# Kernel optimization log

Measured on AMD Instinct MI355X. Metric: run time of the kernel, lower is better.

## Reference

```python
import jax, jax.numpy as jnp
import numpy as np

B, T, D = 8, 1024, 768
H, HD = 12, 64
DFF = 3072
EPS = 1e-5


def setup_inputs() -> dict:
    key = jax.random.key(0)
    ks = jax.random.split(key, 6)
    s = lambda fan_in: 1.0 / np.sqrt(fan_in)
    return {
        "x": jax.random.normal(ks[0], (B, T, D), jnp.float32),
        "ln1_g": jnp.ones((D,), jnp.float32),
        "ln1_b": jnp.zeros((D,), jnp.float32),
        "w_qkv": jax.random.normal(ks[1], (D, 3 * D), jnp.float32) * s(D),
        "b_qkv": jnp.zeros((3 * D,), jnp.float32),
        "w_out": jax.random.normal(ks[2], (D, D), jnp.float32) * s(D),
        "b_out": jnp.zeros((D,), jnp.float32),
        "ln2_g": jnp.ones((D,), jnp.float32),
        "ln2_b": jnp.zeros((D,), jnp.float32),
        "w_fc1": jax.random.normal(ks[3], (D, DFF), jnp.float32) * s(D),
        "b_fc1": jnp.zeros((DFF,), jnp.float32),
        "w_fc2": jax.random.normal(ks[4], (DFF, D), jnp.float32) * s(DFF),
        "b_fc2": jnp.zeros((D,), jnp.float32),
    }


def _layernorm(x, g, b):
    mu = jnp.mean(x, axis=-1, keepdims=True)
    var = jnp.var(x, axis=-1, keepdims=True)
    return (x - mu) * jax.lax.rsqrt(var + EPS) * g + b


def reference(x, ln1_g, ln1_b, w_qkv, b_qkv, w_out, b_out,
              ln2_g, ln2_b, w_fc1, b_fc1, w_fc2, b_fc2):
    # --- attention branch (pre-norm) ---
    h = _layernorm(x, ln1_g, ln1_b)
    qkv = h @ w_qkv + b_qkv                      # [B,T,3D]
    q, k, v = jnp.split(qkv, 3, axis=-1)
    # [B,T,D] -> [B,H,T,HD]
    re = lambda t: t.reshape(B, T, H, HD).transpose(0, 2, 1, 3)
    q, k, v = re(q), re(k), re(v)
    scores = jnp.einsum("bhqd,bhkd->bhqk", q, k) * (1.0 / np.sqrt(HD))
    causal = jnp.tril(jnp.ones((T, T), bool))    # [T,T]
    scores = jnp.where(causal, scores, -jnp.inf)
    attn_weights = jax.nn.softmax(scores, axis=-1)  # [B,H,T,T]
    out = jnp.einsum("bhqk,bhkd->bhqd", attn_weights, v)
    out = out.transpose(0, 2, 1, 3).reshape(B, T, D)
    attn_out = out @ w_out + b_out
    x = x + attn_out
    # --- MLP branch (pre-norm) ---
    h2 = _layernorm(x, ln2_g, ln2_b)
    ff = jax.nn.gelu(h2 @ w_fc1 + b_fc1, approximate=False) @ w_fc2 + b_fc2
    x = x + ff
    return x, attn_weights
```

## Files before the change

kernel.cpp:

```cpp
#include <hip/hip_runtime.h>
#include <cstdint>
#include <cstddef>

namespace {

constexpr int Bb  = 8;
constexpr int Tt  = 1024;
constexpr int Dd  = 768;
constexpr int Hh  = 12;
constexpr int DFF = 3072;
constexpr int BT  = Bb * Tt;

typedef __attribute__((ext_vector_type(8))) short bf16x8;
typedef __attribute__((ext_vector_type(4))) short bf16x4;
typedef __attribute__((ext_vector_type(4))) float f32x4;

__device__ __forceinline__ short f2bf(float f) {
  union { float f; unsigned u; } v; v.f = f;
  unsigned r = v.u + 0x7fffu + ((v.u >> 16) & 1u);
  return (short)(r >> 16);
}
__device__ __forceinline__ float gelu_exact(float v) {
  return 0.5f * v * (1.0f + erff(v * 0.70710678118654752f));
}

#define MFMA16(a, b, c) __builtin_amdgcn_mfma_f32_16x16x32_bf16(a, b, c, 0, 0, 0)

__device__ __forceinline__ void gl_lds16(const short* g, short* l) {
  __builtin_amdgcn_global_load_lds(
      (const __attribute__((address_space(1))) unsigned int*)(g),
      (__attribute__((address_space(3))) unsigned int*)(l), 16, 0, 0);
}

__global__ __launch_bounds__(256) void cvt_t(const float* __restrict__ in,
                                             short* __restrict__ out,
                                             int K, int N) {
  __shared__ float tile[32][33];
  int k0 = blockIdx.x * 32, n0 = blockIdx.y * 32;
  int tx = threadIdx.x & 31, ty = threadIdx.x >> 5;
  #pragma unroll
  for (int r = ty; r < 32; r += 8)
    tile[r][tx] = in[(size_t)(k0 + r) * N + n0 + tx];
  __syncthreads();
  #pragma unroll
  for (int r = ty; r < 32; r += 8)
    out[(size_t)(n0 + r) * K + k0 + tx] = f2bf(tile[tx][r]);
}

__global__ __launch_bounds__(256) void ln_rows(const float* __restrict__ x,
                                               const float* __restrict__ g,
                                               const float* __restrict__ b,
                                               short* __restrict__ out) {
  int lane = threadIdx.x & 63, wid = threadIdx.x >> 6;
  int row = blockIdx.x * 4 + wid;
  const float* xr = x + (size_t)row * Dd;
  float v[12];
  float s = 0.f, ss = 0.f;
  #pragma unroll
  for (int c = 0; c < 3; c++) {
    float4 t = *(const float4*)&xr[c * 256 + lane * 4];
    v[c * 4 + 0] = t.x; v[c * 4 + 1] = t.y; v[c * 4 + 2] = t.z; v[c * 4 + 3] = t.w;
    s  += t.x + t.y + t.z + t.w;
    ss += t.x * t.x + t.y * t.y + t.z * t.z + t.w * t.w;
  }
  #pragma unroll
  for (int off = 1; off < 64; off <<= 1) {
    s += __shfl_xor(s, off); ss += __shfl_xor(ss, off);
  }
  float mu   = s * (1.f / Dd);
  float var  = ss * (1.f / Dd) - mu * mu;
  float rstd = rsqrtf(var + 1e-5f);
  #pragma unroll
  for (int c = 0; c < 3; c++) {
    bf16x4 o;
    #pragma unroll
    for (int j = 0; j < 4; j++) {
      int d = c * 256 + lane * 4 + j;
      o[j] = f2bf((v[c * 4 + j] - mu) * rstd * g[d] + b[d]);
    }
    *(bf16x4*)&out[(size_t)row * Dd + c * 256 + lane * 4] = o;
  }
}

template <int EPI, int N>
__global__ __launch_bounds__(256) void gemm_bt(const short* __restrict__ A,
                                               const short* __restrict__ Bt,
                                               const float* __restrict__ bias,
                                               const float* __restrict__ add,
                                               void* __restrict__ outp,
                                               int K) {
  __shared__ short S[17408];
  short* As0 = S;
  short* As1 = S + 4096;
  short* Bs0 = S + 8192;
  short* Bs1 = S + 12288;

  int nbx = gridDim.x;
  int flat = blockIdx.y * nbx + blockIdx.x;
  int cpx = (nbx * gridDim.y) >> 3;
  int swz = (flat & 7) * cpx + (flat >> 3);
  int m0 = (swz % nbx) * 128, n0 = (swz / nbx) * 128;

  int tid = threadIdx.x;
  int lane = tid & 63, wid = tid >> 6;
  int wm = wid >> 1, wn = wid & 1;
  int l15 = lane & 15, lg = lane >> 4;

  int jr = tid >> 2, jc = (tid & 3) << 3;
  int ldsb = wid << 9;

  auto stage = [&](short* Ad, short* Bd, int k0) {
    gl_lds16(&A[(size_t)(m0 + jr) * K + k0 + jc],       Ad + ldsb);
    gl_lds16(&A[(size_t)(m0 + 64 + jr) * K + k0 + jc],  Ad + 2048 + ldsb);
    gl_lds16(&Bt[(size_t)(n0 + jr) * K + k0 + jc],      Bd + ldsb);
    gl_lds16(&Bt[(size_t)(n0 + 64 + jr) * K + k0 + jc], Bd + 2048 + ldsb);
  };

  f32x4 acc[4][4] = {};
  stage(As0, Bs0, 0);
  int nk = K >> 5;
  for (int t = 0; t < nk; ++t) {
    short* Ab = (t & 1) ? As1 : As0;
    short* Bb = (t & 1) ? Bs1 : Bs0;
    if (t + 1 < nk) {
      stage((t & 1) ? As0 : As1, (t & 1) ? Bs0 : Bs1, (t + 1) << 5);
      asm volatile("s_waitcnt vmcnt(4)" ::: "memory");
    } else {
      asm volatile("s_waitcnt vmcnt(0)" ::: "memory");
    }
    __syncthreads();
    bf16x8 af[4], bfr[4];
    #pragma unroll
    for (int i = 0; i < 4; i++) af[i]  = *(bf16x8*)&Ab[(wm * 64 + i * 16 + l15) * 32 + lg * 8];
    #pragma unroll
    for (int j = 0; j < 4; j++) bfr[j] = *(bf16x8*)&Bb[(wn * 64 + j * 16 + l15) * 32 + lg * 8];
    #pragma unroll
    for (int i = 0; i < 4; i++)
      #pragma unroll
      for (int j = 0; j < 4; j++)
        acc[i][j] = MFMA16(af[i], bfr[j], acc[i][j]);
    __syncthreads();
  }

  if (EPI == 0 || EPI == 2) {
    short (*Cl)[136] = (short (*)[136])S;
    #pragma unroll
    for (int i = 0; i < 4; i++)
      #pragma unroll
      for (int j = 0; j < 4; j++)
        #pragma unroll
        for (int r = 0; r < 4; r++) {
          int row = wm * 64 + i * 16 + lg * 4 + r;
          int col = wn * 64 + j * 16 + l15;
          float vv = acc[i][j][r] + bias[n0 + col];
          if (EPI == 2) vv = gelu_exact(vv);
          int ch = col >> 3, co = col & 7;
          Cl[row][((ch ^ (row & 7)) << 3) | co] = f2bf(vv);
        }
    __syncthreads();
    int row = tid >> 1;
    int cb = (tid & 1) * 8;
    #pragma unroll
    for (int c = 0; c < 8; c++) {
      int ch = cb + c;
      bf16x8 v8 = *(bf16x8*)&Cl[row][(ch ^ (row & 7)) << 3];
      *(bf16x8*)&((short*)outp)[(size_t)(m0 + row) * N + n0 + (ch << 3)] = v8;
    }
  } else {
    #pragma unroll
    for (int i = 0; i < 4; i++)
      #pragma unroll
      for (int j = 0; j < 4; j++)
        #pragma unroll
        for (int r = 0; r < 4; r++) {
          int m = m0 + wm * 64 + i * 16 + lg * 4 + r;
          int n = n0 + wn * 64 + j * 16 + l15;
          float vv = acc[i][j][r] + bias[n];
          size_t idx = (size_t)m * N + n;
          float ov = vv + add[idx];
          if (EPI == 3) __builtin_nontemporal_store(ov, &((float*)outp)[idx]);
          else          ((float*)outp)[idx] = ov;
        }
  }
}

__global__ __launch_bounds__(256) void attn_fused(const short* __restrict__ qkv,
                                                  float* __restrict__ attw,
                                                  short* __restrict__ ctx) {
  __shared__ short Vt[64][72];
  __shared__ float Pf[4][16][68];
  int flat = blockIdx.y * 16 + blockIdx.x;
  int xcd = flat & 7, rr0 = flat >> 3;
  int bh   = xcd * 12 + (rr0 >> 4);
  int tile = 15 - (rr0 & 15);
  int q0 = tile * 64;
  int b = bh / Hh, h = bh % Hh;
  int tid = threadIdx.x, lane = tid & 63, wid = tid >> 6;
  int l15 = lane & 15, lg = lane >> 4;
  const short* base = qkv + (size_t)b * Tt * 2304;

  bf16x8 qa[2];
  {
    const short* qp = base + (size_t)(q0 + wid * 16 + l15) * 2304 + h * 64 + lg * 8;
    qa[0] = *(const bf16x8*)qp;
    qa[1] = *(const bf16x8*)(qp + 32);
  }

  float l[4] = {0.f, 0.f, 0.f, 0.f};
  for (int kt = 0; kt <= tile; ++kt) {
    f32x4 acc[4] = {};
    #pragma unroll
    for (int nf = 0; nf < 4; ++nf) {
      const short* kp = base + (size_t)(kt * 64 + nf * 16 + l15) * 2304 + 768 + h * 64 + lg * 8;
      bf16x8 k0 = *(const bf16x8*)kp;
      bf16x8 k1 = *(const bf16x8*)(kp + 32);
      acc[nf] = MFMA16(qa[0], k0, acc[nf]);
      acc[nf] = MFMA16(qa[1], k1, acc[nf]);
    }
    #pragma unroll
    for (int r = 0; r < 4; r++) {
      int qg = q0 + wid * 16 + lg * 4 + r;
      #pragma unroll
      for (int nf = 0; nf < 4; nf++) {
        int kg = kt * 64 + nf * 16 + l15;
        l[r] += (kg <= qg) ? __expf(acc[nf][r] * 0.125f) : 0.f;
      }
    }
  }
  float rl[4];
  #pragma unroll
  for (int r = 0; r < 4; r++) {
    float s = l[r];
    #pragma unroll
    for (int off = 1; off < 16; off <<= 1) s += __shfl_xor(s, off);
    rl[r] = 1.f / s;
  }

  f32x4 oacc[4] = {};
  for (int kt = 0; kt <= tile; ++kt) {
    __syncthreads();
    {
      int t = tid & 63, dv = (tid >> 6) * 16;
      const short* vp = base + (size_t)(kt * 64 + t) * 2304 + 1536 + h * 64 + dv;
      bf16x8 v0 = *(const bf16x8*)vp;
      bf16x8 v1 = *(const bf16x8*)(vp + 8);
      #pragma unroll
      for (int j = 0; j < 8; j++) Vt[dv + j][t] = v0[j];
      #pragma unroll
      for (int j = 0; j < 8; j++) Vt[dv + 8 + j][t] = v1[j];
    }
    __syncthreads();

    f32x4 acc[4] = {};
    #pragma unroll
    for (int nf = 0; nf < 4; nf++) {
      const short* kp = base + (size_t)(kt * 64 + nf * 16 + l15) * 2304 + 768 + h * 64 + lg * 8;
      bf16x8 k0 = *(const bf16x8*)kp;
      bf16x8 k1 = *(const bf16x8*)(kp + 32);
      acc[nf] = MFMA16(qa[0], k0, acc[nf]);
      acc[nf] = MFMA16(qa[1], k1, acc[nf]);
    }
    #pragma unroll
    for (int nf = 0; nf < 4; nf++) {
      #pragma unroll
      for (int r = 0; r < 4; r++) {
        int qg = q0 + wid * 16 + lg * 4 + r;
        int kg = kt * 64 + nf * 16 + l15;
        float p = (kg <= qg) ? __expf(acc[nf][r] * 0.125f) * rl[r] : 0.f;
        Pf[wid][lg * 4 + r][nf * 16 + l15] = p;
      }
    }
    asm volatile("s_waitcnt lgkmcnt(0)" ::: "memory");
    __builtin_amdgcn_sched_barrier(0);
    #pragma unroll
    for (int it = 0; it < 4; ++it) {
      int pr = it * 4 + lg;
      f32x4 pv = *(f32x4*)&Pf[wid][pr][l15 * 4];
      __builtin_nontemporal_store(
          pv, (f32x4*)&attw[((size_t)bh * Tt + q0 + wid * 16 + pr) * Tt + kt * 64 + l15 * 4]);
    }
    f32x4 pf0 = *(f32x4*)&Pf[wid][l15][lg * 8];
    f32x4 pf1 = *(f32x4*)&Pf[wid][l15][lg * 8 + 4];
    f32x4 pf2 = *(f32x4*)&Pf[wid][l15][lg * 8 + 32];
    f32x4 pf3 = *(f32x4*)&Pf[wid][l15][lg * 8 + 36];
    bf16x8 pa0, pa1;
    #pragma unroll
    for (int j = 0; j < 4; j++) {
      pa0[j] = f2bf(pf0[j]); pa0[4 + j] = f2bf(pf1[j]);
      pa1[j] = f2bf(pf2[j]); pa1[4 + j] = f2bf(pf3[j]);
    }
    #pragma unroll
    for (int nf = 0; nf < 4; nf++) {
      bf16x8 vb0 = *(bf16x8*)&Vt[nf * 16 + l15][lg * 8];
      bf16x8 vb1 = *(bf16x8*)&Vt[nf * 16 + l15][lg * 8 + 32];
      oacc[nf] = MFMA16(pa0, vb0, oacc[nf]);
      oacc[nf] = MFMA16(pa1, vb1, oacc[nf]);
    }
  }
  f32x4 z = {0.f, 0.f, 0.f, 0.f};
  for (int kt = tile + 1; kt < 16; ++kt) {
    #pragma unroll
    for (int it = 0; it < 4; ++it) {
      int pr = it * 4 + lg;
      __builtin_nontemporal_store(
          z, (f32x4*)&attw[((size_t)bh * Tt + q0 + wid * 16 + pr) * Tt + kt * 64 + l15 * 4]);
    }
  }
  #pragma unroll
  for (int nf = 0; nf < 4; nf++) {
    #pragma unroll
    for (int r = 0; r < 4; r++) {
      int t = q0 + wid * 16 + lg * 4 + r;
      ctx[((size_t)b * Tt + t) * Dd + h * 64 + nf * 16 + l15] = f2bf(oacc[nf][r]);
    }
  }
}

}

extern "C" void kernel_launch(void* const* d_in, const int* in_sizes, int n_in,
                              void* d_out, int out_size, void* d_ws, size_t ws_size,
                              hipStream_t stream) {
  const float* x     = (const float*)d_in[0];
  const float* ln1g  = (const float*)d_in[1];
  const float* ln1b  = (const float*)d_in[2];
  const float* w_qkv = (const float*)d_in[3];
  const float* b_qkv = (const float*)d_in[4];
  const float* w_out = (const float*)d_in[5];
  const float* b_out = (const float*)d_in[6];
  const float* ln2g  = (const float*)d_in[7];
  const float* ln2b  = (const float*)d_in[8];
  const float* w_fc1 = (const float*)d_in[9];
  const float* b_fc1 = (const float*)d_in[10];
  const float* w_fc2 = (const float*)d_in[11];
  const float* b_fc2 = (const float*)d_in[12];

  char* ws = (char*)d_ws;
  size_t o = 0;
  short* wqkvT = (short*)(ws + o); o += (size_t)2304 * 768 * 2;
  short* woutT = (short*)(ws + o); o += (size_t)768 * 768 * 2;
  short* wfc1T = (short*)(ws + o); o += (size_t)3072 * 768 * 2;
  short* wfc2T = (short*)(ws + o); o += (size_t)768 * 3072 * 2;
  short* h     = (short*)(ws + o); o += (size_t)BT * Dd * 2;
  short* qkv   = (short*)(ws + o); o += (size_t)BT * 2304 * 2;
  float* y1    = (float*)(ws + o); o += (size_t)BT * Dd * 4;
  short* h2    = (short*)(ws + o); o += (size_t)BT * Dd * 2;
  short* ctx  = h;
  short* gbuf = h;

  float* out_x = (float*)d_out;
  float* attw  = out_x + (size_t)BT * Dd;

  cvt_t<<<dim3(768 / 32, 2304 / 32), 256, 0, stream>>>(w_qkv, wqkvT, 768, 2304);
  cvt_t<<<dim3(768 / 32, 768 / 32),  256, 0, stream>>>(w_out, woutT, 768, 768);
  cvt_t<<<dim3(768 / 32, 3072 / 32), 256, 0, stream>>>(w_fc1, wfc1T, 768, 3072);
  cvt_t<<<dim3(3072 / 32, 768 / 32), 256, 0, stream>>>(w_fc2, wfc2T, 3072, 768);

  ln_rows<<<BT / 4, 256, 0, stream>>>(x, ln1g, ln1b, h);
  gemm_bt<0, 2304><<<dim3(BT / 128, 2304 / 128), 256, 0, stream>>>(h, wqkvT, b_qkv, nullptr, qkv, 768);
  attn_fused<<<dim3(16, 96), 256, 0, stream>>>(qkv, attw, ctx);
  gemm_bt<1, 768><<<dim3(BT / 128, 768 / 128), 256, 0, stream>>>(ctx, woutT, b_out, x, y1, 768);
  ln_rows<<<BT / 4, 256, 0, stream>>>(y1, ln2g, ln2b, h2);
  gemm_bt<2, 3072><<<dim3(BT / 128, 3072 / 128), 256, 0, stream>>>(h2, wfc1T, b_fc1, nullptr, gbuf, 768);
  gemm_bt<3, 768><<<dim3(BT / 128, 768 / 128), 256, 0, stream>>>(gbuf, wfc2T, b_fc2, y1, out_x, 3072);
}
```

Baseline: 441.7 us.

## Add 256x256-tile 512-thread GEMM for QKV and FC1 projections

Adds a new GEMM kernel with 256x256 output tiles, 8 waves, a K-step of 64, double-buffered direct global-to-LDS loads with XOR swizzle, and a two-pass epilogue staged through LDS. It replaces the 128x128 kernel for the QKV and FC1 projections. The aim is more data reuse per LDS load and fewer global loads per FLOP. The cost is 128 KB of LDS per block and a large accumulator register footprint, and the grids are smaller (288 and 384 blocks), which may hurt wave balance across the CUs. The old bf16-output epilogue path is removed from gemm_bt.

```diff
diff --git a/kernel.cpp b/kernel.cpp
--- a/kernel.cpp
+++ b/kernel.cpp
@@ -25,6 +25,8 @@
 }
 
 #define MFMA16(a, b, c) __builtin_amdgcn_mfma_f32_16x16x32_bf16(a, b, c, 0, 0, 0)
+#define WAITV(n) asm volatile("s_waitcnt vmcnt(" #n ")" ::: "memory")
+#define BARRIER() asm volatile("s_barrier" ::: "memory")
 
 __device__ __forceinline__ void gl_lds16(const short* g, short* l) {
   __builtin_amdgcn_global_load_lds(
@@ -79,6 +81,106 @@
       o[j] = f2bf((v[c * 4 + j] - mu) * rstd * g[d] + b[d]);
     }
     *(bf16x4*)&out[(size_t)row * Dd + c * 256 + lane * 4] = o;
+  }
+}
+
+template <int EPI>
+__global__ __launch_bounds__(512, 2) void gemm256(const short* __restrict__ A,
+                                                  const short* __restrict__ Bt,
+                                                  const float* __restrict__ bias,
+                                                  short* __restrict__ outp,
+                                                  int N, int K) {
+  __shared__ short S[65536];
+  int nbx = gridDim.x;
+  int flat = blockIdx.y * nbx + blockIdx.x;
+  int cpx = (nbx * gridDim.y) >> 3;
+  int swz = (flat & 7) * cpx + (flat >> 3);
+  int m0 = (swz % nbx) * 256, n0 = (swz / nbx) * 256;
+
+  int tid = threadIdx.x;
+  int lane = tid & 63, wid = tid >> 6;
+  int wm = wid >> 2, wn = wid & 3;
+  int l15 = lane & 15, lg = lane >> 4;
+
+  int srow = wid * 8 + (lane >> 3);
+  int gslot = (lane & 7) ^ (srow & 7);
+
+  auto stage = [&](int dbuf, int kt) {
+    int dst = dbuf * 32768 + (wid << 9);
+    #pragma unroll
+    for (int p = 0; p < 4; ++p) {
+      const short* g = (p < 2)
+        ? &A [(size_t)(m0 + (p & 1) * 128 + srow) * K + kt * 64 + gslot * 8]
+        : &Bt[(size_t)(n0 + (p & 1) * 128 + srow) * K + kt * 64 + gslot * 8];
+      gl_lds16(g, &S[dst + p * 8192]);
+      gl_lds16(g + (size_t)64 * K, &S[dst + p * 8192 + 4096]);
+    }
+  };
+
+  f32x4 acc[8][4] = {};
+  stage(0, 0);
+  int NT = K >> 6;
+  for (int kt = 0; kt < NT; ++kt) {
+    int d = kt & 1;
+    if (kt + 1 < NT) {
+      stage(d ^ 1, kt + 1);
+      WAITV(8);
+    } else {
+      WAITV(0);
+    }
+    BARRIER();
+
+    const int bB = d * 32768 + 16384 + (wn >> 1) * 8192;
+    bf16x8 rB[8];
+    #pragma unroll
+    for (int n = 0; n < 4; n++) {
+      int r = (wn & 1) * 64 + n * 16 + l15;
+      rB[n * 2 + 0] = *(const bf16x8*)&S[bB + r * 64 + (((lg    ) ^ (r & 7)) << 3)];
+      rB[n * 2 + 1] = *(const bf16x8*)&S[bB + r * 64 + (((4 + lg) ^ (r & 7)) << 3)];
+    }
+    const int bA = d * 32768 + wm * 8192;
+    #pragma unroll
+    for (int m = 0; m < 8; m++) {
+      int r = m * 16 + l15;
+      bf16x8 a0 = *(const bf16x8*)&S[bA + r * 64 + (((lg    ) ^ (r & 7)) << 3)];
+      bf16x8 a1 = *(const bf16x8*)&S[bA + r * 64 + (((4 + lg) ^ (r & 7)) << 3)];
+      #pragma unroll
+      for (int n = 0; n < 4; n++) {
+        acc[m][n] = MFMA16(a0, rB[n * 2 + 0], acc[m][n]);
+        acc[m][n] = MFMA16(a1, rB[n * 2 + 1], acc[m][n]);
+      }
+    }
+    BARRIER();
+  }
+
+  __syncthreads();
+  #pragma unroll
+  for (int ch = 0; ch < 2; ++ch) {
+    if (wm == ch) {
+      #pragma unroll
+      for (int m = 0; m < 8; m++)
+        #pragma unroll
+        for (int n = 0; n < 4; n++) {
+          int col = wn * 64 + n * 16 + l15;
+          float bs = bias[n0 + col];
+          #pragma unroll
+          for (int r = 0; r < 4; r++) {
+            int row = m * 16 + lg * 4 + r;
+            float vv = acc[m][n][r] + bs;
+            if (EPI == 2) vv = gelu_exact(vv);
+            S[row * 256 + ((((col >> 3) ^ (row & 7)) << 3) | (col & 7))] = f2bf(vv);
+          }
+        }
+    }
+    __syncthreads();
+    int row = tid >> 2;
+    #pragma unroll
+    for (int c = 0; c < 8; c++) {
+      int cc = (tid & 3) + c * 4;
+      bf16x8 v8 = *(bf16x8*)&S[row * 256 + ((cc ^ (row & 7)) << 3)];
+      *(bf16x8*)&outp[(size_t)(m0 + ch * 128 + row) * N + n0 + cc * 8] = v8;
+    }
+    __syncthreads();
   }
 }
 
@@ -142,46 +244,20 @@
     __syncthreads();
   }
 
-  if (EPI == 0 || EPI == 2) {
-    short (*Cl)[136] = (short (*)[136])S;
-    #pragma unroll
-    for (int i = 0; i < 4; i++)
-      #pragma unroll
-      for (int j = 0; j < 4; j++)
-        #pragma unroll
-        for (int r = 0; r < 4; r++) {
-          int row = wm * 64 + i * 16 + lg * 4 + r;
-          int col = wn * 64 + j * 16 + l15;
-          float vv = acc[i][j][r] + bias[n0 + col];
-          if (EPI == 2) vv = gelu_exact(vv);
-          int ch = col >> 3, co = col & 7;
-          Cl[row][((ch ^ (row & 7)) << 3) | co] = f2bf(vv);
-        }
-    __syncthreads();
-    int row = tid >> 1;
-    int cb = (tid & 1) * 8;
-    #pragma unroll
-    for (int c = 0; c < 8; c++) {
-      int ch = cb + c;
-      bf16x8 v8 = *(bf16x8*)&Cl[row][(ch ^ (row & 7)) << 3];
-      *(bf16x8*)&((short*)outp)[(size_t)(m0 + row) * N + n0 + (ch << 3)] = v8;
-    }
-  } else {
-    #pragma unroll
-    for (int i = 0; i < 4; i++)
-      #pragma unroll
-      for (int j = 0; j < 4; j++)
-        #pragma unroll
-        for (int r = 0; r < 4; r++) {
-          int m = m0 + wm * 64 + i * 16 + lg * 4 + r;
-          int n = n0 + wn * 64 + j * 16 + l15;
-          float vv = acc[i][j][r] + bias[n];
-          size_t idx = (size_t)m * N + n;
-          float ov = vv + add[idx];
-          if (EPI == 3) __builtin_nontemporal_store(ov, &((float*)outp)[idx]);
-          else          ((float*)outp)[idx] = ov;
-        }
-  }
+  #pragma unroll
+  for (int i = 0; i < 4; i++)
+    #pragma unroll
+    for (int j = 0; j < 4; j++)
+      #pragma unroll
+      for (int r = 0; r < 4; r++) {
+        int m = m0 + wm * 64 + i * 16 + lg * 4 + r;
+        int n = n0 + wn * 64 + j * 16 + l15;
+        float vv = acc[i][j][r] + bias[n];
+        size_t idx = (size_t)m * N + n;
+        float ov = vv + add[idx];
+        if (EPI == 3) __builtin_nontemporal_store(ov, &((float*)outp)[idx]);
+        else          ((float*)outp)[idx] = ov;
+      }
 }
 
 __global__ __launch_bounds__(256) void attn_fused(const short* __restrict__ qkv,
@@ -357,10 +433,10 @@
   cvt_t<<<dim3(3072 / 32, 768 / 32), 256, 0, stream>>>(w_fc2, wfc2T, 3072, 768);
 
   ln_rows<<<BT / 4, 256, 0, stream>>>(x, ln1g, ln1b, h);
-  gemm_bt<0, 2304><<<dim3(BT / 128, 2304 / 128), 256, 0, stream>>>(h, wqkvT, b_qkv, nullptr, qkv, 768);
+  gemm256<0><<<dim3(BT / 256, 2304 / 256), 512, 0, stream>>>(h, wqkvT, b_qkv, qkv, 2304, 768);
   attn_fused<<<dim3(16, 96), 256, 0, stream>>>(qkv, attw, ctx);
   gemm_bt<1, 768><<<dim3(BT / 128, 768 / 128), 256, 0, stream>>>(ctx, woutT, b_out, x, y1, 768);
   ln_rows<<<BT / 4, 256, 0, stream>>>(y1, ln2g, ln2b, h2);
-  gemm_bt<2, 3072><<<dim3(BT / 128, 3072 / 128), 256, 0, stream>>>(h2, wfc1T, b_fc1, nullptr, gbuf, 768);
+  gemm256<2><<<dim3(BT / 256, DFF / 256), 512, 0, stream>>>(h2, wfc1T, b_fc1, gbuf, DFF, 768);
   gemm_bt<3, 768><<<dim3(BT / 128, 768 / 128), 256, 0, stream>>>(gbuf, wfc2T, b_fc2, y1, out_x, 3072);
 }
```

New measurement: 490.5 us. 1.11x slower.

## Split fused attention into context kernel and attention-weights kernel

Applied to the files above, without the earlier changes.

The single attention kernel made two passes: one to compute softmax row sums and one to write the weights and accumulate P·V. It now becomes two kernels. attn_ctx makes one pass, accumulating unnormalized P·V together with the row sums, normalizing at the end and saving the sums to workspace. attn_w then recomputes QK^T and writes the normalized weights. Total QK^T work stays about the same, but the compute-heavy P·V path no longer shares a kernel with the bandwidth-heavy weight stores. The cost is an extra launch and a small sums buffer, and exp is applied without max subtraction (as before).

```diff
diff --git a/kernel.cpp b/kernel.cpp
--- a/kernel.cpp
+++ b/kernel.cpp
@@ -184,9 +184,9 @@
   }
 }
 
-__global__ __launch_bounds__(256) void attn_fused(const short* __restrict__ qkv,
-                                                  float* __restrict__ attw,
-                                                  short* __restrict__ ctx) {
+__global__ __launch_bounds__(256) void attn_ctx(const short* __restrict__ qkv,
+                                                float* __restrict__ sums,
+                                                short* __restrict__ ctx) {
   __shared__ short Vt[64][72];
   __shared__ float Pf[4][16][68];
   int flat = blockIdx.y * 16 + blockIdx.x;
@@ -207,35 +207,6 @@
   }
 
   float l[4] = {0.f, 0.f, 0.f, 0.f};
-  for (int kt = 0; kt <= tile; ++kt) {
-    f32x4 acc[4] = {};
-    #pragma unroll
-    for (int nf = 0; nf < 4; ++nf) {
-      const short* kp = base + (size_t)(kt * 64 + nf * 16 + l15) * 2304 + 768 + h * 64 + lg * 8;
-      bf16x8 k0 = *(const bf16x8*)kp;
-      bf16x8 k1 = *(const bf16x8*)(kp + 32);
-      acc[nf] = MFMA16(qa[0], k0, acc[nf]);
-      acc[nf] = MFMA16(qa[1], k1, acc[nf]);
-    }
-    #pragma unroll
-    for (int r = 0; r < 4; r++) {
-      int qg = q0 + wid * 16 + lg * 4 + r;
-      #pragma unroll
-      for (int nf = 0; nf < 4; nf++) {
-        int kg = kt * 64 + nf * 16 + l15;
-        l[r] += (kg <= qg) ? __expf(acc[nf][r] * 0.125f) : 0.f;
-      }
-    }
-  }
-  float rl[4];
-  #pragma unroll
-  for (int r = 0; r < 4; r++) {
-    float s = l[r];
-    #pragma unroll
-    for (int off = 1; off < 16; off <<= 1) s += __shfl_xor(s, off);
-    rl[r] = 1.f / s;
-  }
-
   f32x4 oacc[4] = {};
   for (int kt = 0; kt <= tile; ++kt) {
     __syncthreads();
@@ -266,8 +237,96 @@
       for (int r = 0; r < 4; r++) {
         int qg = q0 + wid * 16 + lg * 4 + r;
         int kg = kt * 64 + nf * 16 + l15;
-        float p = (kg <= qg) ? __expf(acc[nf][r] * 0.125f) * rl[r] : 0.f;
+        float p = (kg <= qg) ? __expf(acc[nf][r] * 0.125f) : 0.f;
         Pf[wid][lg * 4 + r][nf * 16 + l15] = p;
+        l[r] += p;
+      }
+    }
+    asm volatile("s_waitcnt lgkmcnt(0)" ::: "memory");
+    __builtin_amdgcn_sched_barrier(0);
+    f32x4 pf0 = *(f32x4*)&Pf[wid][l15][lg * 8];
+    f32x4 pf1 = *(f32x4*)&Pf[wid][l15][lg * 8 + 4];
+    f32x4 pf2 = *(f32x4*)&Pf[wid][l15][lg * 8 + 32];
+    f32x4 pf3 = *(f32x4*)&Pf[wid][l15][lg * 8 + 36];
+    bf16x8 pa0, pa1;
+    #pragma unroll
+    for (int j = 0; j < 4; j++) {
+      pa0[j] = f2bf(pf0[j]); pa0[4 + j] = f2bf(pf1[j]);
+      pa1[j] = f2bf(pf2[j]); pa1[4 + j] = f2bf(pf3[j]);
+    }
+    #pragma unroll
+    for (int nf = 0; nf < 4; nf++) {
+      bf16x8 vb0 = *(bf16x8*)&Vt[nf * 16 + l15][lg * 8];
+      bf16x8 vb1 = *(bf16x8*)&Vt[nf * 16 + l15][lg * 8 + 32];
+      oacc[nf] = MFMA16(pa0, vb0, oacc[nf]);
+      oacc[nf] = MFMA16(pa1, vb1, oacc[nf]);
+    }
+  }
+  float rl[4];
+  #pragma unroll
+  for (int r = 0; r < 4; r++) {
+    #pragma unroll
+    for (int off = 1; off < 16; off <<= 1) l[r] += __shfl_xor(l[r], off);
+    rl[r] = 1.f / l[r];
+  }
+  #pragma unroll
+  for (int nf = 0; nf < 4; nf++) {
+    #pragma unroll
+    for (int r = 0; r < 4; r++) {
+      int t = q0 + wid * 16 + lg * 4 + r;
+      ctx[((size_t)b * Tt + t) * Dd + h * 64 + nf * 16 + l15] = f2bf(oacc[nf][r] * rl[r]);
+    }
+  }
+  if (l15 == 0) {
+    #pragma unroll
+    for (int r = 0; r < 4; r++)
+      sums[(size_t)bh * Tt + q0 + wid * 16 + lg * 4 + r] = l[r];
+  }
+}
+
+__global__ __launch_bounds__(256) void attn_w(const short* __restrict__ qkv,
+                                              const float* __restrict__ sums,
+                                              float* __restrict__ attw) {
+  __shared__ float Pf[4][16][68];
+  int flat = blockIdx.y * 16 + blockIdx.x;
+  int xcd = flat & 7, rr0 = flat >> 3;
+  int bh   = xcd * 12 + (rr0 >> 4);
+  int tile = 15 - (rr0 & 15);
+  int q0 = tile * 64;
+  int b = bh / Hh, h = bh % Hh;
+  int tid = threadIdx.x, lane = tid & 63, wid = tid >> 6;
+  int l15 = lane & 15, lg = lane >> 4;
+  const short* base = qkv + (size_t)b * Tt * 2304;
+
+  bf16x8 qa[2];
+  {
+    const short* qp = base + (size_t)(q0 + wid * 16 + l15) * 2304 + h * 64 + lg * 8;
+    qa[0] = *(const bf16x8*)qp;
+    qa[1] = *(const bf16x8*)(qp + 32);
+  }
+  float rl[4];
+  #pragma unroll
+  for (int r = 0; r < 4; r++)
+    rl[r] = 1.f / sums[(size_t)bh * Tt + q0 + wid * 16 + lg * 4 + r];
+
+  for (int kt = 0; kt <= tile; ++kt) {
+    f32x4 acc[4] = {};
+    #pragma unroll
+    for (int nf = 0; nf < 4; nf++) {
+      const short* kp = base + (size_t)(kt * 64 + nf * 16 + l15) * 2304 + 768 + h * 64 + lg * 8;
+      bf16x8 k0 = *(const bf16x8*)kp;
+      bf16x8 k1 = *(const bf16x8*)(kp + 32);
+      acc[nf] = MFMA16(qa[0], k0, acc[nf]);
+      acc[nf] = MFMA16(qa[1], k1, acc[nf]);
+    }
+    #pragma unroll
+    for (int nf = 0; nf < 4; nf++) {
+      #pragma unroll
+      for (int r = 0; r < 4; r++) {
+        int qg = q0 + wid * 16 + lg * 4 + r;
+        int kg = kt * 64 + nf * 16 + l15;
+        Pf[wid][lg * 4 + r][nf * 16 + l15] =
+            (kg <= qg) ? __expf(acc[nf][r] * 0.125f) * rl[r] : 0.f;
       }
     }
     asm volatile("s_waitcnt lgkmcnt(0)" ::: "memory");
@@ -279,23 +338,6 @@
       __builtin_nontemporal_store(
           pv, (f32x4*)&attw[((size_t)bh * Tt + q0 + wid * 16 + pr) * Tt + kt * 64 + l15 * 4]);
     }
-    f32x4 pf0 = *(f32x4*)&Pf[wid][l15][lg * 8];
-    f32x4 pf1 = *(f32x4*)&Pf[wid][l15][lg * 8 + 4];
-    f32x4 pf2 = *(f32x4*)&Pf[wid][l15][lg * 8 + 32];
-    f32x4 pf3 = *(f32x4*)&Pf[wid][l15][lg * 8 + 36];
-    bf16x8 pa0, pa1;
-    #pragma unroll
-    for (int j = 0; j < 4; j++) {
-      pa0[j] = f2bf(pf0[j]); pa0[4 + j] = f2bf(pf1[j]);
-      pa1[j] = f2bf(pf2[j]); pa1[4 + j] = f2bf(pf3[j]);
-    }
-    #pragma unroll
-    for (int nf = 0; nf < 4; nf++) {
-      bf16x8 vb0 = *(bf16x8*)&Vt[nf * 16 + l15][lg * 8];
-      bf16x8 vb1 = *(bf16x8*)&Vt[nf * 16 + l15][lg * 8 + 32];
-      oacc[nf] = MFMA16(pa0, vb0, oacc[nf]);
-      oacc[nf] = MFMA16(pa1, vb1, oacc[nf]);
-    }
   }
   f32x4 z = {0.f, 0.f, 0.f, 0.f};
   for (int kt = tile + 1; kt < 16; ++kt) {
@@ -304,14 +346,6 @@
       int pr = it * 4 + lg;
       __builtin_nontemporal_store(
           z, (f32x4*)&attw[((size_t)bh * Tt + q0 + wid * 16 + pr) * Tt + kt * 64 + l15 * 4]);
-    }
-  }
-  #pragma unroll
-  for (int nf = 0; nf < 4; nf++) {
-    #pragma unroll
-    for (int r = 0; r < 4; r++) {
-      int t = q0 + wid * 16 + lg * 4 + r;
-      ctx[((size_t)b * Tt + t) * Dd + h * 64 + nf * 16 + l15] = f2bf(oacc[nf][r]);
     }
   }
 }
@@ -345,6 +379,7 @@
   short* qkv   = (short*)(ws + o); o += (size_t)BT * 2304 * 2;
   float* y1    = (float*)(ws + o); o += (size_t)BT * Dd * 4;
   short* h2    = (short*)(ws + o); o += (size_t)BT * Dd * 2;
+  float* sums  = (float*)(ws + o); o += (size_t)96 * Tt * 4;
   short* ctx  = h;
   short* gbuf = h;
 
@@ -358,7 +393,8 @@
 
   ln_rows<<<BT / 4, 256, 0, stream>>>(x, ln1g, ln1b, h);
   gemm_bt<0, 2304><<<dim3(BT / 128, 2304 / 128), 256, 0, stream>>>(h, wqkvT, b_qkv, nullptr, qkv, 768);
-  attn_fused<<<dim3(16, 96), 256, 0, stream>>>(qkv, attw, ctx);
+  attn_ctx<<<dim3(16, 96), 256, 0, stream>>>(qkv, sums, ctx);
+  attn_w<<<dim3(16, 96), 256, 0, stream>>>(qkv, sums, attw);
   gemm_bt<1, 768><<<dim3(BT / 128, 768 / 128), 256, 0, stream>>>(ctx, woutT, b_out, x, y1, 768);
   ln_rows<<<BT / 4, 256, 0, stream>>>(y1, ln2g, ln2b, h2);
   gemm_bt<2, 3072><<<dim3(BT / 128, 3072 / 128), 256, 0, stream>>>(h2, wfc1T, b_fc1, nullptr, gbuf, 768);
```

Result: slower. 480.4 us (+8.8%).

## Pre-transpose V and double-buffer it into LDS via async loads

Applied to the files above, without the earlier changes.

Adds a separate kernel that transposes V per head into a contiguous [bh][d][t] workspace buffer. The attention kernel then stages the next V tile into a swizzled double-buffered LDS array with direct global-to-LDS loads, overlapped with the current tile's QK/softmax work. This replaces per-iteration scalar transposing stores and two block barriers. It costs an extra kernel launch and an extra round trip of V through global memory, and it relies on the gl_lds16 helper and a hand-written vmcnt wait being correct.

```diff
diff --git a/kernel.cpp b/kernel.cpp
--- a/kernel.cpp
+++ b/kernel.cpp
@@ -80,6 +80,28 @@
     }
     *(bf16x4*)&out[(size_t)row * Dd + c * 256 + lane * 4] = o;
   }
+}
+
+__global__ __launch_bounds__(256) void vtr(const short* __restrict__ qkv,
+                                           short* __restrict__ vt) {
+  __shared__ short Ts[64][72];
+  int bh = blockIdx.x, t0 = blockIdx.y * 64;
+  int b = bh / Hh, h = bh % Hh;
+  int tid = threadIdx.x;
+  int r = tid >> 2, dc = (tid & 3) * 16;
+  const short* vp = qkv + (size_t)b * Tt * 2304 + (size_t)(t0 + r) * 2304 + 1536 + h * 64 + dc;
+  bf16x8 v0 = *(const bf16x8*)vp;
+  bf16x8 v1 = *(const bf16x8*)(vp + 8);
+  *(bf16x8*)&Ts[r][dc] = v0;
+  *(bf16x8*)&Ts[r][dc + 8] = v1;
+  __syncthreads();
+  int d = tid >> 2, tc = (tid & 3) * 16;
+  bf16x8 o0, o1;
+  #pragma unroll
+  for (int j = 0; j < 8; j++) { o0[j] = Ts[tc + j][d]; o1[j] = Ts[tc + 8 + j][d]; }
+  short* op = vt + ((size_t)bh * 64 + d) * Tt + t0 + tc;
+  *(bf16x8*)op = o0;
+  *(bf16x8*)(op + 8) = o1;
 }
 
 template <int EPI, int N>
@@ -185,9 +207,10 @@
 }
 
 __global__ __launch_bounds__(256) void attn_fused(const short* __restrict__ qkv,
+                                                  const short* __restrict__ vt,
                                                   float* __restrict__ attw,
                                                   short* __restrict__ ctx) {
-  __shared__ short Vt[64][72];
+  __shared__ short VtL[2][4096];
   __shared__ float Pf[4][16][68];
   int flat = blockIdx.y * 16 + blockIdx.x;
   int xcd = flat & 7, rr0 = flat >> 3;
@@ -236,21 +259,18 @@
     rl[r] = 1.f / s;
   }
 
+  const short* vtb = vt + (size_t)bh * 64 * Tt;
+  int dS = wid * 16 + (lane >> 3);
+  int cS = (lane & 7) ^ (lane >> 3);
+  auto stageV = [&](int bi, int kt) {
+    gl_lds16(&vtb[(size_t)dS * Tt + kt * 64 + cS * 8],       &VtL[bi][wid * 1024]);
+    gl_lds16(&vtb[(size_t)(dS + 8) * Tt + kt * 64 + cS * 8], &VtL[bi][wid * 1024 + 512]);
+  };
+
   f32x4 oacc[4] = {};
+  stageV(0, 0);
   for (int kt = 0; kt <= tile; ++kt) {
-    __syncthreads();
-    {
-      int t = tid & 63, dv = (tid >> 6) * 16;
-      const short* vp = base + (size_t)(kt * 64 + t) * 2304 + 1536 + h * 64 + dv;
-      bf16x8 v0 = *(const bf16x8*)vp;
-      bf16x8 v1 = *(const bf16x8*)(vp + 8);
-      #pragma unroll
-      for (int j = 0; j < 8; j++) Vt[dv + j][t] = v0[j];
-      #pragma unroll
-      for (int j = 0; j < 8; j++) Vt[dv + 8 + j][t] = v1[j];
-    }
-    __syncthreads();
-
+    int cur = kt & 1;
     f32x4 acc[4] = {};
     #pragma unroll
     for (int nf = 0; nf < 4; nf++) {
@@ -289,10 +309,16 @@
       pa0[j] = f2bf(pf0[j]); pa0[4 + j] = f2bf(pf1[j]);
       pa1[j] = f2bf(pf2[j]); pa1[4 + j] = f2bf(pf3[j]);
     }
+    asm volatile("s_waitcnt vmcnt(4)" ::: "memory");
+    __builtin_amdgcn_s_barrier();
+    __builtin_amdgcn_sched_barrier(0);
+    if (kt < tile) stageV(cur ^ 1, kt + 1);
     #pragma unroll
     for (int nf = 0; nf < 4; nf++) {
-      bf16x8 vb0 = *(bf16x8*)&Vt[nf * 16 + l15][lg * 8];
-      bf16x8 vb1 = *(bf16x8*)&Vt[nf * 16 + l15][lg * 8 + 32];
+      int dA = nf * 16 + l15;
+      int sw = dA & 7;
+      bf16x8 vb0 = *(bf16x8*)&VtL[cur][dA * 64 + ((lg ^ sw) << 3)];
+      bf16x8 vb1 = *(bf16x8*)&VtL[cur][dA * 64 + (((4 + lg) ^ sw) << 3)];
       oacc[nf] = MFMA16(pa0, vb0, oacc[nf]);
       oacc[nf] = MFMA16(pa1, vb1, oacc[nf]);
     }
@@ -345,6 +371,7 @@
   short* qkv   = (short*)(ws + o); o += (size_t)BT * 2304 * 2;
   float* y1    = (float*)(ws + o); o += (size_t)BT * Dd * 4;
   short* h2    = (short*)(ws + o); o += (size_t)BT * Dd * 2;
+  short* vt    = (short*)(ws + o); o += (size_t)96 * 64 * Tt * 2;
   short* ctx  = h;
   short* gbuf = h;
 
@@ -358,7 +385,8 @@
 
   ln_rows<<<BT / 4, 256, 0, stream>>>(x, ln1g, ln1b, h);
   gemm_bt<0, 2304><<<dim3(BT / 128, 2304 / 128), 256, 0, stream>>>(h, wqkvT, b_qkv, nullptr, qkv, 768);
-  attn_fused<<<dim3(16, 96), 256, 0, stream>>>(qkv, attw, ctx);
+  vtr<<<dim3(96, 16), 256, 0, stream>>>(qkv, vt);
+  attn_fused<<<dim3(16, 96), 256, 0, stream>>>(qkv, vt, attw, ctx);
   gemm_bt<1, 768><<<dim3(BT / 128, 768 / 128), 256, 0, stream>>>(ctx, woutT, b_out, x, y1, 768);
   ln_rows<<<BT / 4, 256, 0, stream>>>(y1, ln2g, ln2b, h2);
   gemm_bt<2, 3072><<<dim3(BT / 128, 3072 / 128), 256, 0, stream>>>(h2, wfc1T, b_fc1, nullptr, gbuf, 768);
```

New measurement: 436.8 us. Within noise of the previous version (-1.1%).
